# Kernel tuning notes

Hardware: AMD Instinct MI355X
Metric: run time of the kernel (lower is better)

Reference implementation:

```python
import jax, jax.numpy as jnp
import numpy as np

NO_EDGE_OFFSET_T_NORM = 2.0    # pushes no_edge above data range so min() ignores it
NO_EDGE_OFFSET_T_CONORM = -1.0 # pushes no_edge below data range so max() ignores it


def _daa_layer(x, sel, is_t_norm):
    """One DAALayer with a single operator for all nodes (LAYER_WISE init).

    x:   [B, in_features] float
    sel: [out_features, in_features] int, edge type per (node, input):
         0 = no_edge (value 0 + operator-dependent offset), 1 = normal_edge (value x)
    """
    off = NO_EDGE_OFFSET_T_NORM if is_t_norm else NO_EDGE_OFFSET_T_CONORM
    # [B, out, in]: gather edge values per node according to hard routing
    vals = jnp.where(sel[None, :, :] == 1, x[:, None, :], jnp.float32(off))
    # t-norm 'min' / t-conorm 'max' reduction over incoming edges
    return vals.min(axis=-1) if is_t_norm else vals.max(axis=-1)


def setup_inputs() -> dict:
    key = jax.random.key(0)
    k1, k2, k3 = jax.random.split(key, 3)
    B, IN, HID = 256, 1024, 512
    x = jax.random.uniform(k1, (B, IN), dtype=jnp.float32)
    # hard gumbel-softmax over all-ones logits == uniform edge-type choice
    sel0 = jax.random.randint(k2, (HID, IN), 0, 2)  # layer 0: 1024 -> 512
    sel1 = jax.random.randint(k3, (IN, HID), 0, 2)  # layer 1: 512 -> 1024
    return {"x": x, "sel0": sel0, "sel1": sel1}


def reference(x, sel0, sel1):
    h = _daa_layer(x, sel0, True)    # layer 0: T_Norm.min on all nodes
    out = _daa_layer(h, sel1, False)  # layer 1: T_Conorm.max on all nodes
    return out
```

## Files before the change

kernel.cpp:

```cpp
#include <hip/hip_runtime.h>


#define NB 256

__global__ __launch_bounds__(256) void pack_all(
    const float* __restrict__ x,    float4* __restrict__ xT4,
    const int*   __restrict__ sel0, float4* __restrict__ a0h,
    const int*   __restrict__ sel1, float4* __restrict__ a1h)
{
    const int t = blockIdx.x * 256 + threadIdx.x;
    const float pinf = __builtin_inff();

    {
        const int j = t >> 8, i4 = t & 255;
        const int srow = (j >> 2) * 8 + 4 + (j & 3);
        const int4 v = ((const int4*)sel0)[srow * 256 + i4];
        a0h[t] = make_float4(v.x ? 0.f : pinf, v.y ? 0.f : pinf,
                             v.z ? 0.f : pinf, v.w ? 0.f : pinf);
    }
    {
        const int j = t >> 7, i4 = t & 127;
        const int srow = (j >> 2) * 8 + 4 + (j & 3);
        const int4 v = ((const int4*)sel1)[srow * 128 + i4];
        a1h[t] = make_float4(v.x ? 0.f : -pinf, v.y ? 0.f : -pinf,
                             v.z ? 0.f : -pinf, v.w ? 0.f : -pinf);
    }

    if (blockIdx.x < 64) {
        __shared__ float tt[64][65];
        const int bx = blockIdx.x % 16;
        const int by = blockIdx.x / 16;
        const int i0 = bx * 64, b0 = by * 64;

        const int li = threadIdx.x & 63;
        const int lb = threadIdx.x >> 6;
#pragma unroll
        for (int r = 0; r < 64; r += 4)
            tt[lb + r][li] = x[(size_t)(b0 + lb + r) * 1024 + i0 + li];
        __syncthreads();

        const int sb = threadIdx.x & 63;
        const int si = threadIdx.x >> 6;
#pragma unroll
        for (int p = 0; p < 16; p += 4) {
            const int i4 = si + p;
            float4 v = make_float4(tt[sb][4 * i4 + 0], tt[sb][4 * i4 + 1],
                                   tt[sb][4 * i4 + 2], tt[sb][4 * i4 + 3]);
            xT4[(size_t)(i0 / 4 + i4) * NB + b0 + sb] = v;
        }
    }
}

template<int INF, int S, int MW, bool ISMIN, bool TOUT>
__global__ __launch_bounds__(64 * S, MW) void daa_layer(
    const float4* __restrict__ inT4,
    const int*    __restrict__ sel,
    const float4* __restrict__ agh,
    float* __restrict__ out, int OUTF)
{
    constexpr int C4  = INF / 4 / S;
    constexpr int R4  = INF / 4;
    const int tid  = threadIdx.x;
    const int lane = tid & 63;
    const int s    = __builtin_amdgcn_readfirstlane(tid >> 6);
    const int bch  = blockIdx.x & 3;
    const int o0   = (blockIdx.x >> 2) * 8;
    const int b    = bch * 64 + lane;
    const float off = ISMIN ? 2.0f : -1.0f;
    const float inf = ISMIN ? __builtin_inff() : -__builtin_inff();

    __shared__ float4 uni[2048];

    if (tid < 4 * R4) {
        const int4 v = ((const int4*)sel)[(size_t)o0 * R4 + tid];
        uni[tid] = make_float4(v.x ? 0.f : inf, v.y ? 0.f : inf,
                               v.z ? 0.f : inf, v.w ? 0.f : inf);
    }
    __syncthreads();

    float acc[8];
#pragma unroll
    for (int u = 0; u < 8; ++u) acc[u] = off;

    const float4* __restrict__ xp = inT4 + (size_t)(s * C4) * NB + b;
    const float4* __restrict__ aL = uni + s * C4;
    const float4* __restrict__ aG = agh + ((size_t)(o0 >> 3) * 4) * R4 + s * C4;

#define MM(A, X, AV)                                                   \
    do {                                                               \
        if (ISMIN) {                                                   \
            A = fminf(fminf(A, (X).x + (AV).x), (X).y + (AV).y);       \
            A = fminf(fminf(A, (X).z + (AV).z), (X).w + (AV).w);       \
        } else {                                                       \
            A = fmaxf(fmaxf(A, (X).x + (AV).x), (X).y + (AV).y);       \
            A = fmaxf(fmaxf(A, (X).z + (AV).z), (X).w + (AV).w);       \
        }                                                              \
    } while (0)

    float4 xa = xp[0];
    for (int c = 0; c < C4; ++c) {
        float4 nx = xa;
        if (c + 1 < C4) nx = xp[(size_t)(c + 1) * NB];
#pragma unroll
        for (int u = 0; u < 4; ++u) {
            const float4 av = aL[u * R4 + c];
            MM(acc[u], xa, av);
        }
#pragma unroll
        for (int u = 0; u < 4; ++u) {
            const float4 av = aG[u * R4 + c];
            MM(acc[4 + u], xa, av);
        }
        xa = nx;
    }
#undef MM

    __syncthreads();
    float* redf = (float*)uni;
#pragma unroll
    for (int u = 0; u < 8; ++u) redf[(s * 8 + u) * 64 + lane] = acc[u];
    __syncthreads();

    if (tid < 512) {
        const int u = tid >> 6, ln = tid & 63;
        float v = redf[u * 64 + ln];
#pragma unroll
        for (int ss = 1; ss < S; ++ss) {
            const float q = redf[(ss * 8 + u) * 64 + ln];
            v = ISMIN ? fminf(v, q) : fmaxf(v, q);
        }
        redf[u * 64 + ln] = v;
    }
    __syncthreads();

    if (tid < 64) {
        const int bb = bch * 64 + tid;
        const float4 lo = make_float4(redf[0 * 64 + tid], redf[1 * 64 + tid],
                                      redf[2 * 64 + tid], redf[3 * 64 + tid]);
        const float4 hi = make_float4(redf[4 * 64 + tid], redf[5 * 64 + tid],
                                      redf[6 * 64 + tid], redf[7 * 64 + tid]);
        if (TOUT) {
            ((float4*)out)[(size_t)(o0 >> 2) * NB + bb]       = lo;
            ((float4*)out)[((size_t)(o0 >> 2) + 1) * NB + bb] = hi;
        } else {
            float4* p = (float4*)(out + (size_t)bb * OUTF + o0);
            p[0] = lo; p[1] = hi;
        }
    }
}

extern "C" void kernel_launch(void* const* d_in, const int* in_sizes, int n_in,
                              void* d_out, int out_size, void* d_ws, size_t ws_size,
                              hipStream_t stream) {
    const float* x    = (const float*)d_in[0];
    const int*   sel0 = (const int*)d_in[1];
    const int*   sel1 = (const int*)d_in[2];
    float* out = (float*)d_out;

    char* ws = (char*)d_ws;
    float4* xT4 = (float4*)ws;
    float*  hT  = (float*)(ws + (1 << 20));
    float4* a0h = (float4*)(ws + 3 * (1 << 19));
    float4* a1h = (float4*)(ws + 5 * (1 << 19));

    pack_all<<<256, 256, 0, stream>>>(x, xT4, sel0, a0h, sel1, a1h);
    daa_layer<1024, 16, 4, true,  true ><<<256, 1024, 0, stream>>>(
        xT4, sel0, a0h, hT, 512);
    daa_layer< 512, 16, 8, false, false><<<512, 1024, 0, stream>>>(
        (const float4*)hT, sel1, a1h, out, 1024);
}
```

Before: 25.35 us.

## Fuse pack and both DAA layers into one persistent kernel with grid barriers

Merges the pack kernel and the two layer kernels into a single 256-block launch, separated by software grid barriers built on atomic counters that are reset with a memset each call. Layer 1 work is done by each block processing two virtual blocks in sequence. The aim is to remove the overhead and drain gaps of multiple kernel launches. In exchange it adds a memset, spin-wait barriers that depend on all 256 blocks of 1024 threads being resident at once, and lower parallelism in the second layer.

```diff
diff --git a/kernel.cpp b/kernel.cpp
--- a/kernel.cpp
+++ b/kernel.cpp
@@ -3,74 +3,39 @@
 
 #define NB 256
 
-__global__ __launch_bounds__(256) void pack_all(
-    const float* __restrict__ x,    float4* __restrict__ xT4,
-    const int*   __restrict__ sel0, float4* __restrict__ a0h,
-    const int*   __restrict__ sel1, float4* __restrict__ a1h)
-{
-    const int t = blockIdx.x * 256 + threadIdx.x;
-    const float pinf = __builtin_inff();
-
-    {
-        const int j = t >> 8, i4 = t & 255;
-        const int srow = (j >> 2) * 8 + 4 + (j & 3);
-        const int4 v = ((const int4*)sel0)[srow * 256 + i4];
-        a0h[t] = make_float4(v.x ? 0.f : pinf, v.y ? 0.f : pinf,
-                             v.z ? 0.f : pinf, v.w ? 0.f : pinf);
+__device__ __forceinline__ void gridbar(unsigned* cnt, unsigned target) {
+    __syncthreads();
+    if (threadIdx.x == 0) {
+        __threadfence();
+        __hip_atomic_fetch_add(cnt, 1u, __ATOMIC_ACQ_REL,
+                               __HIP_MEMORY_SCOPE_AGENT);
+        while (__hip_atomic_load(cnt, __ATOMIC_ACQUIRE,
+                                 __HIP_MEMORY_SCOPE_AGENT) < target)
+            __builtin_amdgcn_s_sleep(2);
     }
-    {
-        const int j = t >> 7, i4 = t & 127;
-        const int srow = (j >> 2) * 8 + 4 + (j & 3);
-        const int4 v = ((const int4*)sel1)[srow * 128 + i4];
-        a1h[t] = make_float4(v.x ? 0.f : -pinf, v.y ? 0.f : -pinf,
-                             v.z ? 0.f : -pinf, v.w ? 0.f : -pinf);
-    }
-
-    if (blockIdx.x < 64) {
-        __shared__ float tt[64][65];
-        const int bx = blockIdx.x % 16;
-        const int by = blockIdx.x / 16;
-        const int i0 = bx * 64, b0 = by * 64;
-
-        const int li = threadIdx.x & 63;
-        const int lb = threadIdx.x >> 6;
-#pragma unroll
-        for (int r = 0; r < 64; r += 4)
-            tt[lb + r][li] = x[(size_t)(b0 + lb + r) * 1024 + i0 + li];
-        __syncthreads();
-
-        const int sb = threadIdx.x & 63;
-        const int si = threadIdx.x >> 6;
-#pragma unroll
-        for (int p = 0; p < 16; p += 4) {
-            const int i4 = si + p;
-            float4 v = make_float4(tt[sb][4 * i4 + 0], tt[sb][4 * i4 + 1],
-                                   tt[sb][4 * i4 + 2], tt[sb][4 * i4 + 3]);
-            xT4[(size_t)(i0 / 4 + i4) * NB + b0 + sb] = v;
-        }
-    }
+    __syncthreads();
 }
 
-template<int INF, int S, int MW, bool ISMIN, bool TOUT>
-__global__ __launch_bounds__(64 * S, MW) void daa_layer(
+template<int INF, bool ISMIN, bool TOUT>
+__device__ __forceinline__ void daa_phase(
     const float4* __restrict__ inT4,
     const int*    __restrict__ sel,
     const float4* __restrict__ agh,
-    float* __restrict__ out, int OUTF)
+    float* __restrict__ out, int OUTF, int vblk, float4* uni)
 {
-    constexpr int C4  = INF / 4 / S;
-    constexpr int R4  = INF / 4;
+    constexpr int S  = 16;
+    constexpr int C4 = INF / 4 / S;
+    constexpr int R4 = INF / 4;
     const int tid  = threadIdx.x;
     const int lane = tid & 63;
     const int s    = __builtin_amdgcn_readfirstlane(tid >> 6);
-    const int bch  = blockIdx.x & 3;
-    const int o0   = (blockIdx.x >> 2) * 8;
+    const int bch  = vblk & 3;
+    const int o0   = (vblk >> 2) * 8;
     const int b    = bch * 64 + lane;
     const float off = ISMIN ? 2.0f : -1.0f;
     const float inf = ISMIN ? __builtin_inff() : -__builtin_inff();
 
-    __shared__ float4 uni[2048];
-
+    __syncthreads();
     if (tid < 4 * R4) {
         const int4 v = ((const int4*)sel)[(size_t)o0 * R4 + tid];
         uni[tid] = make_float4(v.x ? 0.f : inf, v.y ? 0.f : inf,
@@ -149,6 +114,64 @@
     }
 }
 
+__global__ __launch_bounds__(1024, 4) void daa_fused(
+    const float* __restrict__ x,
+    const int*   __restrict__ sel0, const int* __restrict__ sel1,
+    float4* __restrict__ xT4, float* __restrict__ hT,
+    float4* __restrict__ a0h, float4* __restrict__ a1h,
+    unsigned* __restrict__ bars, float* __restrict__ out)
+{
+    __shared__ float4 uni[2048];
+    const int blk = blockIdx.x, tid = threadIdx.x;
+    const unsigned nblk = gridDim.x;
+
+    {
+        const int g = blk * 1024 + tid;
+        const float pinf = __builtin_inff();
+        if (g < 65536) {
+            const int j = g >> 8, i4 = g & 255;
+            const int srow = (j >> 2) * 8 + 4 + (j & 3);
+            const int4 v = ((const int4*)sel0)[srow * 256 + i4];
+            a0h[g] = make_float4(v.x ? 0.f : pinf, v.y ? 0.f : pinf,
+                                 v.z ? 0.f : pinf, v.w ? 0.f : pinf);
+        } else if (g < 131072) {
+            const int t4 = g - 65536;
+            const int j = t4 >> 7, i4 = t4 & 127;
+            const int srow = (j >> 2) * 8 + 4 + (j & 3);
+            const int4 v = ((const int4*)sel1)[srow * 128 + i4];
+            a1h[t4] = make_float4(v.x ? 0.f : -pinf, v.y ? 0.f : -pinf,
+                                  v.z ? 0.f : -pinf, v.w ? 0.f : -pinf);
+        }
+    }
+
+    {
+        float* tmp = (float*)uni;
+        const int i0 = (blk & 15) * 64, b0 = (blk >> 4) * 16;
+        const int r = tid >> 6, c = tid & 63;
+        tmp[r * 65 + c] = x[(size_t)(b0 + r) * 1024 + i0 + c];
+        __syncthreads();
+        if (tid < 256) {
+            const int i4 = tid >> 4, bb = tid & 15;
+            xT4[(size_t)(i0 / 4 + i4) * NB + b0 + bb] =
+                make_float4(tmp[bb * 65 + 4 * i4 + 0],
+                            tmp[bb * 65 + 4 * i4 + 1],
+                            tmp[bb * 65 + 4 * i4 + 2],
+                            tmp[bb * 65 + 4 * i4 + 3]);
+        }
+    }
+
+    gridbar(bars + 0, nblk);
+
+    daa_phase<1024, true, true>(xT4, sel0, a0h, hT, 512, blk, uni);
+
+    gridbar(bars + 32, nblk);
+
+    daa_phase<512, false, false>((const float4*)hT, sel1, a1h, out, 1024,
+                                 2 * blk + 0, uni);
+    daa_phase<512, false, false>((const float4*)hT, sel1, a1h, out, 1024,
+                                 2 * blk + 1, uni);
+}
+
 extern "C" void kernel_launch(void* const* d_in, const int* in_sizes, int n_in,
                               void* d_out, int out_size, void* d_ws, size_t ws_size,
                               hipStream_t stream) {
@@ -158,14 +181,14 @@
     float* out = (float*)d_out;
 
     char* ws = (char*)d_ws;
-    float4* xT4 = (float4*)ws;
-    float*  hT  = (float*)(ws + (1 << 20));
-    float4* a0h = (float4*)(ws + 3 * (1 << 19));
-    float4* a1h = (float4*)(ws + 5 * (1 << 19));
+    float4*   xT4  = (float4*)ws;
+    float*    hT   = (float*)(ws + (1 << 20));
+    float4*   a0h  = (float4*)(ws + 3 * (1 << 19));
+    float4*   a1h  = (float4*)(ws + 5 * (1 << 19));
+    unsigned* bars = (unsigned*)(ws + (4 << 20));
 
-    pack_all<<<256, 256, 0, stream>>>(x, xT4, sel0, a0h, sel1, a1h);
-    daa_layer<1024, 16, 4, true,  true ><<<256, 1024, 0, stream>>>(
-        xT4, sel0, a0h, hT, 512);
-    daa_layer< 512, 16, 8, false, false><<<512, 1024, 0, stream>>>(
-        (const float4*)hT, sel1, a1h, out, 1024);
+    hipMemsetAsync(bars, 0, 256, stream);
+
+    daa_fused<<<256, 1024, 0, stream>>>(x, sel0, sel1, xT4, hT, a0h, a1h,
+                                        bars, out);
 }
```

After: 83.64 us. 230% more time.
